# Optimization experiments

Hardware: AMD Instinct MI355X
Metric: run time of the kernel (lower is better)

## Reference

```python
import jax, jax.numpy as jnp
import numpy as np

N = 50000
E = 600000
IN_DIM = 256
OUT_DIM = 128
SCALE = 1.8
K = 2
ALPHA = 0.15
EPS = 1e-12  # matches F.normalize eps


def setup_inputs() -> dict:
    key = jax.random.key(0)
    k1, k2, k3, k4 = jax.random.split(key, 4)
    x = jax.random.normal(k1, (N, IN_DIM), dtype=jnp.float32)
    edge_index = jax.random.randint(k2, (2, E), 0, N, dtype=jnp.int64)
    # nn.Linear params (Kaiming-uniform-ish init scale)
    lim = 1.0 / np.sqrt(IN_DIM)
    W = jax.random.uniform(k3, (OUT_DIM, IN_DIM), dtype=jnp.float32, minval=-lim, maxval=lim)
    b = jax.random.uniform(k4, (OUT_DIM,), dtype=jnp.float32, minval=-lim, maxval=lim)
    return {"x": x, "edge_index": edge_index, "W": W, "b": b}


def _gcn_norm(edge_index, num_nodes):
    # add self loops, symmetric normalization D^-1/2 A D^-1/2
    loops = jnp.arange(num_nodes, dtype=edge_index.dtype)
    row = jnp.concatenate([edge_index[0], loops])  # source
    col = jnp.concatenate([edge_index[1], loops])  # target
    deg = jax.ops.segment_sum(jnp.ones_like(col, dtype=jnp.float32), col,
                              num_segments=num_nodes)
    dinv = jnp.where(deg > 0, jax.lax.rsqrt(deg), 0.0)
    w = dinv[row] * dinv[col]
    return row, col, w


def reference(x, edge_index, W, b):
    # linear
    h = x @ W.T + b  # [N, OUT_DIM]
    # L2 normalize over feature dim, then scale
    nrm = jnp.sqrt(jnp.sum(h * h, axis=1, keepdims=True))
    h = h / jnp.maximum(nrm, EPS) * SCALE
    # APPNP propagation (eval mode: edge dropout disabled)
    row, col, w = _gcn_norm(edge_index, N)
    z = h
    for _ in range(K):
        msg = w[:, None] * z[row]  # gather + weight, [E+N, OUT_DIM]
        agg = jax.ops.segment_sum(msg, col, num_segments=N)
        z = (1.0 - ALPHA) * agg + ALPHA * h
    return z
```

## Files before the change

### kernel.cpp

```cpp
#include <hip/hip_runtime.h>
#include <hip/hip_bf16.h>

#define NNODES 50000
#define IN_DIM 256
#define OUT_DIM 128
#define SCALE 1.8f
#define ALPHA 0.15f
#define DSTRIDE 64

typedef unsigned short ushort_t;
typedef __attribute__((ext_vector_type(8))) _Float16 f16x8;
typedef __attribute__((ext_vector_type(4))) float f32x4;


__device__ __forceinline__ unsigned short f2bf_rne(float f) {
    unsigned int u = __float_as_uint(f);
    unsigned int r = u + 0x7fffu + ((u >> 16) & 1u);
    return (unsigned short)(r >> 16);
}

__device__ __forceinline__ float2 bf2_to_f2(unsigned int p) {
    float2 f;
    f.x = __uint_as_float(p << 16);
    f.y = __uint_as_float(p & 0xffff0000u);
    return f;
}

__device__ __forceinline__ unsigned int f2_to_bf2(float x, float y) {
    return (unsigned int)f2bf_rne(x) | ((unsigned int)f2bf_rne(y) << 16);
}

__device__ __forceinline__ unsigned short f2h(float f) {
    _Float16 h = (_Float16)f;
    return *(unsigned short*)&h;
}


__global__ void init_kernel(const float* __restrict__ W, ushort_t* __restrict__ Whf,
                            int* __restrict__ cnt) {
    int i = blockIdx.x * 256 + threadIdx.x;
    if (i < 50048) cnt[i] = 0;
    if (i < OUT_DIM * IN_DIM) Whf[i] = f2h(W[i]);
}


__global__ void fill_kernel(const int* __restrict__ row, const int* __restrict__ col,
                            int* __restrict__ cnt, int* __restrict__ csr, int E) {
    int e = blockIdx.x * blockDim.x + threadIdx.x;
    if (e < E) {
        int c = col[e];
        int p = atomicAdd(&cnt[c], 1);
        if (p < DSTRIDE) csr[c * DSTRIDE + p] = row[e];
    }
}


#define XPAD 264

__global__ void __launch_bounds__(256, 4) gemm_norm_kernel(
        const float* __restrict__ x, const ushort_t* __restrict__ Whf,
        const float* __restrict__ b, const int* __restrict__ cnt,
        ushort_t* __restrict__ s0b) {
    __shared__ __align__(16) ushort_t xh[64][XPAD];

    const int t = threadIdx.x;
    const int wv = t >> 6;
    const int lane = t & 63;
    const int q = lane >> 4;
    const int c = lane & 15;
    const int rowBase = blockIdx.x * 64;

    f16x8 wf[2][8];
    float bias[2];
    #pragma unroll
    for (int j = 0; j < 2; ++j) {
        const size_t base = (size_t)((2 * wv + j) * 16 + c) * IN_DIM + q * 8;
        #pragma unroll
        for (int kt = 0; kt < 8; ++kt)
            wf[j][kt] = *(const f16x8*)(Whf + base + kt * 32);
        bias[j] = b[(2 * wv + j) * 16 + c];
    }

    #pragma unroll
    for (int it = 0; it < 16; ++it) {
        int s = it * 256 + t;
        int r = s >> 6;
        int ks = (s & 63) * 4;
        int grow = rowBase + r;
        float4 v = make_float4(0.f, 0.f, 0.f, 0.f);
        if (grow < NNODES) v = *(const float4*)(x + (size_t)grow * IN_DIM + ks);
        uint2 p;
        p.x = (unsigned int)f2h(v.x) | ((unsigned int)f2h(v.y) << 16);
        p.y = (unsigned int)f2h(v.z) | ((unsigned int)f2h(v.w) << 16);
        *(uint2*)&xh[r][ks] = p;
    }
    __syncthreads();

    f32x4 acc[4][2];
    #pragma unroll
    for (int m = 0; m < 4; ++m)
        #pragma unroll
        for (int j = 0; j < 2; ++j) {
            acc[m][j][0] = bias[j]; acc[m][j][1] = bias[j];
            acc[m][j][2] = bias[j]; acc[m][j][3] = bias[j];
        }

    #pragma unroll
    for (int kt = 0; kt < 8; ++kt) {
        const int kb = kt * 32 + q * 8;
        #pragma unroll
        for (int m = 0; m < 4; ++m) {
            f16x8 a = *(const f16x8*)&xh[m * 16 + c][kb];
            #pragma unroll
            for (int j = 0; j < 2; ++j)
                acc[m][j] = __builtin_amdgcn_mfma_f32_16x16x32_f16(a, wf[j][kt], acc[m][j], 0, 0, 0);
        }
    }

    float psum[4][4];
    #pragma unroll
    for (int m = 0; m < 4; ++m)
        #pragma unroll
        for (int r = 0; r < 4; ++r)
            psum[m][r] = acc[m][0][r] * acc[m][0][r] + acc[m][1][r] * acc[m][1][r];
    #pragma unroll
    for (int mask = 1; mask < 16; mask <<= 1)
        #pragma unroll
        for (int m = 0; m < 4; ++m)
            #pragma unroll
            for (int r = 0; r < 4; ++r)
                psum[m][r] += __shfl_xor(psum[m][r], mask);

    __syncthreads();
    float* red = (float*)&xh[0][0];
    float* scl = red + 64 * 8;
    if (c == 0) {
        #pragma unroll
        for (int m = 0; m < 4; ++m)
            #pragma unroll
            for (int r = 0; r < 4; ++r)
                red[(m * 16 + q * 4 + r) * 8 + wv] = psum[m][r];
    }
    __syncthreads();
    if (t < 64) {
        float s = red[t * 8 + 0] + red[t * 8 + 1] + red[t * 8 + 2] + red[t * 8 + 3];
        float d = rsqrtf((float)(cnt[rowBase + t] + 1));
        scl[t] = d * SCALE / fmaxf(sqrtf(s), 1e-12f);
    }
    __syncthreads();

    #pragma unroll
    for (int m = 0; m < 4; ++m) {
        #pragma unroll
        for (int r = 0; r < 4; ++r) {
            int lrow = m * 16 + q * 4 + r;
            int grow = rowBase + lrow;
            if (grow < NNODES) {
                float sc = scl[lrow];
                #pragma unroll
                for (int j = 0; j < 2; ++j) {
                    float o = acc[m][j][r] * sc;
                    s0b[(size_t)grow * OUT_DIM + (2 * wv + j) * 16 + c] = f2bf_rne(o);
                }
            }
        }
    }
}


__device__ __forceinline__ void acc_row4(float2* a, uint4 v) {
    float2 f0 = bf2_to_f2(v.x), f1 = bf2_to_f2(v.y);
    float2 f2 = bf2_to_f2(v.z), f3 = bf2_to_f2(v.w);
    a[0].x += f0.x; a[0].y += f0.y;
    a[1].x += f1.x; a[1].y += f1.y;
    a[2].x += f2.x; a[2].y += f2.y;
    a[3].x += f3.x; a[3].y += f3.y;
}

template <int FINAL>
__global__ void __launch_bounds__(256) gather_kernel(
        const int* __restrict__ cnt, const int* __restrict__ csr,
        const unsigned int* __restrict__ sin, const unsigned int* __restrict__ s0,
        unsigned int* __restrict__ sout_b, float* __restrict__ out_f) {
    const int wv = threadIdx.x >> 6;
    const int lane = threadIdx.x & 63;
    const int qd = lane >> 4;
    const int d16 = lane & 15;
    const int c = blockIdx.x * 4 + wv;

    const int deg = cnt[c];
    int n = deg;
    if (n > DSTRIDE) n = DSTRIDE;
    int idx = 0;
    if (lane < n) idx = csr[c * DSTRIDE + lane];

    float2 a[4];
    #pragma unroll
    for (int k = 0; k < 4; ++k) a[k] = make_float2(0.f, 0.f);

    int j = 0;
    for (; j + 8 <= n; j += 8) {
        int r0 = __shfl(idx, j + qd);
        int r1 = __shfl(idx, j + 4 + qd);
        uint4 v0 = *(const uint4*)(sin + (size_t)r0 * 64 + d16 * 4);
        uint4 v1 = *(const uint4*)(sin + (size_t)r1 * 64 + d16 * 4);
        acc_row4(a, v0);
        acc_row4(a, v1);
    }
    for (; j < n; j += 4) {
        int jj = j + qd;
        int r0 = __shfl(idx, (jj < n) ? jj : (n - 1));
        if (jj < n) {
            uint4 v0 = *(const uint4*)(sin + (size_t)r0 * 64 + d16 * 4);
            acc_row4(a, v0);
        }
    }

    #pragma unroll
    for (int k = 0; k < 4; ++k) {
        a[k].x += __shfl_xor(a[k].x, 16);
        a[k].y += __shfl_xor(a[k].y, 16);
        a[k].x += __shfl_xor(a[k].x, 32);
        a[k].y += __shfl_xor(a[k].y, 32);
    }

    if (qd == 0) {
        const float degp1 = (float)(deg + 1);
        uint4 zc4 = *(const uint4*)(sin + (size_t)c * 64 + d16 * 4);
        float2 zc[4];
        zc[0] = bf2_to_f2(zc4.x); zc[1] = bf2_to_f2(zc4.y);
        zc[2] = bf2_to_f2(zc4.z); zc[3] = bf2_to_f2(zc4.w);
        #pragma unroll
        for (int k = 0; k < 4; ++k) {
            a[k].x += zc[k].x;
            a[k].y += zc[k].y;
        }
        if (FINAL) {
            float d = rsqrtf(degp1);
            float gx = (1.0f - ALPHA) * d;
            float gy = ALPHA * sqrtf(degp1);
            uint4 z04 = *(const uint4*)(s0 + (size_t)c * 64 + d16 * 4);
            float2 z0[4];
            z0[0] = bf2_to_f2(z04.x); z0[1] = bf2_to_f2(z04.y);
            z0[2] = bf2_to_f2(z04.z); z0[3] = bf2_to_f2(z04.w);
            float4 o0, o1;
            o0.x = gx * a[0].x + gy * z0[0].x;
            o0.y = gx * a[0].y + gy * z0[0].y;
            o0.z = gx * a[1].x + gy * z0[1].x;
            o0.w = gx * a[1].y + gy * z0[1].y;
            o1.x = gx * a[2].x + gy * z0[2].x;
            o1.y = gx * a[2].y + gy * z0[2].y;
            o1.z = gx * a[3].x + gy * z0[3].x;
            o1.w = gx * a[3].y + gy * z0[3].y;
            float* p = out_f + (size_t)c * 128 + d16 * 8;
            *(float4*)(p) = o0;
            *(float4*)(p + 4) = o1;
        } else {
            float qc = (1.0f - ALPHA) / degp1;
            uint4 w;
            w.x = f2_to_bf2(qc * a[0].x + ALPHA * zc[0].x, qc * a[0].y + ALPHA * zc[0].y);
            w.y = f2_to_bf2(qc * a[1].x + ALPHA * zc[1].x, qc * a[1].y + ALPHA * zc[1].y);
            w.z = f2_to_bf2(qc * a[2].x + ALPHA * zc[2].x, qc * a[2].y + ALPHA * zc[2].y);
            w.w = f2_to_bf2(qc * a[3].x + ALPHA * zc[3].x, qc * a[3].y + ALPHA * zc[3].y);
            *(uint4*)(sout_b + (size_t)c * 64 + d16 * 4) = w;
        }
    }
}

extern "C" void kernel_launch(void* const* d_in, const int* in_sizes, int n_in,
                              void* d_out, int out_size, void* d_ws, size_t ws_size,
                              hipStream_t stream) {
    const float* x  = (const float*)d_in[0];
    const int*   ei = (const int*)d_in[1];
    const float* W  = (const float*)d_in[2];
    const float* b  = (const float*)d_in[3];
    float* out = (float*)d_out;

    int E = in_sizes[1] / 2;
    const int* row = ei;
    const int* col = ei + E;

    unsigned int* s0b = (unsigned int*)d_ws;
    unsigned int* s1b = s0b + (size_t)NNODES * 64;
    int* csr = (int*)(s1b + (size_t)NNODES * 64);
    int* cnt = csr + (size_t)NNODES * DSTRIDE;
    ushort_t* Whf = (ushort_t*)(cnt + 50048);

    init_kernel<<<196, 256, 0, stream>>>(W, Whf, cnt);
    fill_kernel<<<(E + 255) / 256, 256, 0, stream>>>(row, col, cnt, csr, E);
    gemm_norm_kernel<<<(NNODES + 63) / 64, 256, 0, stream>>>(x, Whf, b, cnt, (ushort_t*)s0b);
    gather_kernel<0><<<NNODES / 4, 256, 0, stream>>>(cnt, csr, s0b, s0b, s1b, nullptr);
    gather_kernel<1><<<NNODES / 4, 256, 0, stream>>>(cnt, csr, s1b, s0b, nullptr, out);
}
```

Measured before the change: 196.3 us.

## Fuse CSR fill into GEMM launch, defer degree scaling to gather, use 16-bit CSR

The separate init, fill and GEMM kernels are merged into one launch. Extra blocks build the CSR with atomics while the GEMM blocks run independently, and W is converted to fp16 inline instead of in a pre-pass. Because the GEMM no longer needs the degree counts, the source-side D^-1/2 factor moves into the first gather as a per-neighbour rsqrt of cnt. CSR indices are stored as 16-bit values to halve index traffic, which risks truncation since node ids go up to 50000 (below 65536, so they fit). The cost is an extra cnt load per edge in the first gather.

```diff
diff --git a/kernel.cpp b/kernel.cpp
--- a/kernel.cpp
+++ b/kernel.cpp
@@ -7,6 +7,7 @@
 #define SCALE 1.8f
 #define ALPHA 0.15f
 #define DSTRIDE 64
+#define GEMM_BLOCKS 782
 
 typedef unsigned short ushort_t;
 typedef __attribute__((ext_vector_type(8))) _Float16 f16x8;
@@ -36,32 +37,28 @@
 }
 
 
-__global__ void init_kernel(const float* __restrict__ W, ushort_t* __restrict__ Whf,
-                            int* __restrict__ cnt) {
-    int i = blockIdx.x * 256 + threadIdx.x;
-    if (i < 50048) cnt[i] = 0;
-    if (i < OUT_DIM * IN_DIM) Whf[i] = f2h(W[i]);
-}
-
-
-__global__ void fill_kernel(const int* __restrict__ row, const int* __restrict__ col,
-                            int* __restrict__ cnt, int* __restrict__ csr, int E) {
-    int e = blockIdx.x * blockDim.x + threadIdx.x;
-    if (e < E) {
-        int c = col[e];
-        int p = atomicAdd(&cnt[c], 1);
-        if (p < DSTRIDE) csr[c * DSTRIDE + p] = row[e];
-    }
-}
-
-
 #define XPAD 264
 
-__global__ void __launch_bounds__(256, 4) gemm_norm_kernel(
-        const float* __restrict__ x, const ushort_t* __restrict__ Whf,
-        const float* __restrict__ b, const int* __restrict__ cnt,
-        ushort_t* __restrict__ s0b) {
+__global__ void __launch_bounds__(256, 4) prep_gemm_kernel(
+        const float* __restrict__ x, const float* __restrict__ W,
+        const float* __restrict__ b,
+        const int* __restrict__ row, const int* __restrict__ col, int E,
+        int* __restrict__ cnt, ushort_t* __restrict__ csr16,
+        ushort_t* __restrict__ u0b) {
     __shared__ __align__(16) ushort_t xh[64][XPAD];
+
+    if (blockIdx.x >= GEMM_BLOCKS) {
+        int e0 = ((blockIdx.x - GEMM_BLOCKS) * 256 + threadIdx.x) * 2;
+        if (e0 < E) {
+            int2 rr = *(const int2*)(row + e0);
+            int2 cc = *(const int2*)(col + e0);
+            int p0 = atomicAdd(&cnt[cc.x], 1);
+            if (p0 < DSTRIDE) csr16[(size_t)cc.x * DSTRIDE + p0] = (ushort_t)rr.x;
+            int p1 = atomicAdd(&cnt[cc.y], 1);
+            if (p1 < DSTRIDE) csr16[(size_t)cc.y * DSTRIDE + p1] = (ushort_t)rr.y;
+        }
+        return;
+    }
 
     const int t = threadIdx.x;
     const int wv = t >> 6;
@@ -76,8 +73,16 @@
     for (int j = 0; j < 2; ++j) {
         const size_t base = (size_t)((2 * wv + j) * 16 + c) * IN_DIM + q * 8;
         #pragma unroll
-        for (int kt = 0; kt < 8; ++kt)
-            wf[j][kt] = *(const f16x8*)(Whf + base + kt * 32);
+        for (int kt = 0; kt < 8; ++kt) {
+            float4 w0 = *(const float4*)(W + base + kt * 32);
+            float4 w1 = *(const float4*)(W + base + kt * 32 + 4);
+            f16x8 wp;
+            wp[0] = (_Float16)w0.x; wp[1] = (_Float16)w0.y;
+            wp[2] = (_Float16)w0.z; wp[3] = (_Float16)w0.w;
+            wp[4] = (_Float16)w1.x; wp[5] = (_Float16)w1.y;
+            wp[6] = (_Float16)w1.z; wp[7] = (_Float16)w1.w;
+            wf[j][kt] = wp;
+        }
         bias[j] = b[(2 * wv + j) * 16 + c];
     }
 
@@ -144,8 +149,7 @@
     __syncthreads();
     if (t < 64) {
         float s = red[t * 8 + 0] + red[t * 8 + 1] + red[t * 8 + 2] + red[t * 8 + 3];
-        float d = rsqrtf((float)(cnt[rowBase + t] + 1));
-        scl[t] = d * SCALE / fmaxf(sqrtf(s), 1e-12f);
+        scl[t] = SCALE / fmaxf(sqrtf(s), 1e-12f);
     }
     __syncthreads();
 
@@ -160,7 +164,7 @@
                 #pragma unroll
                 for (int j = 0; j < 2; ++j) {
                     float o = acc[m][j][r] * sc;
-                    s0b[(size_t)grow * OUT_DIM + (2 * wv + j) * 16 + c] = f2bf_rne(o);
+                    u0b[(size_t)grow * OUT_DIM + (2 * wv + j) * 16 + c] = f2bf_rne(o);
                 }
             }
         }
@@ -168,19 +172,10 @@
 }
 
 
-__device__ __forceinline__ void acc_row4(float2* a, uint4 v) {
-    float2 f0 = bf2_to_f2(v.x), f1 = bf2_to_f2(v.y);
-    float2 f2 = bf2_to_f2(v.z), f3 = bf2_to_f2(v.w);
-    a[0].x += f0.x; a[0].y += f0.y;
-    a[1].x += f1.x; a[1].y += f1.y;
-    a[2].x += f2.x; a[2].y += f2.y;
-    a[3].x += f3.x; a[3].y += f3.y;
-}
-
 template <int FINAL>
 __global__ void __launch_bounds__(256) gather_kernel(
-        const int* __restrict__ cnt, const int* __restrict__ csr,
-        const unsigned int* __restrict__ sin, const unsigned int* __restrict__ s0,
+        const int* __restrict__ cnt, const ushort_t* __restrict__ csr16,
+        const unsigned int* __restrict__ sin, const unsigned int* __restrict__ u0,
         unsigned int* __restrict__ sout_b, float* __restrict__ out_f) {
     const int wv = threadIdx.x >> 6;
     const int lane = threadIdx.x & 63;
@@ -192,7 +187,7 @@
     int n = deg;
     if (n > DSTRIDE) n = DSTRIDE;
     int idx = 0;
-    if (lane < n) idx = csr[c * DSTRIDE + lane];
+    if (lane < n) idx = (int)csr16[(size_t)c * DSTRIDE + lane];
 
     float2 a[4];
     #pragma unroll
@@ -202,17 +197,43 @@
     for (; j + 8 <= n; j += 8) {
         int r0 = __shfl(idx, j + qd);
         int r1 = __shfl(idx, j + 4 + qd);
+        float sc0 = 1.0f, sc1 = 1.0f;
+        if (!FINAL) {
+            sc0 = rsqrtf((float)(cnt[r0] + 1));
+            sc1 = rsqrtf((float)(cnt[r1] + 1));
+        }
         uint4 v0 = *(const uint4*)(sin + (size_t)r0 * 64 + d16 * 4);
         uint4 v1 = *(const uint4*)(sin + (size_t)r1 * 64 + d16 * 4);
-        acc_row4(a, v0);
-        acc_row4(a, v1);
+        {
+            float2 f0 = bf2_to_f2(v0.x), f1 = bf2_to_f2(v0.y);
+            float2 f2 = bf2_to_f2(v0.z), f3 = bf2_to_f2(v0.w);
+            a[0].x += sc0 * f0.x; a[0].y += sc0 * f0.y;
+            a[1].x += sc0 * f1.x; a[1].y += sc0 * f1.y;
+            a[2].x += sc0 * f2.x; a[2].y += sc0 * f2.y;
+            a[3].x += sc0 * f3.x; a[3].y += sc0 * f3.y;
+        }
+        {
+            float2 f0 = bf2_to_f2(v1.x), f1 = bf2_to_f2(v1.y);
+            float2 f2 = bf2_to_f2(v1.z), f3 = bf2_to_f2(v1.w);
+            a[0].x += sc1 * f0.x; a[0].y += sc1 * f0.y;
+            a[1].x += sc1 * f1.x; a[1].y += sc1 * f1.y;
+            a[2].x += sc1 * f2.x; a[2].y += sc1 * f2.y;
+            a[3].x += sc1 * f3.x; a[3].y += sc1 * f3.y;
+        }
     }
     for (; j < n; j += 4) {
         int jj = j + qd;
-        int r0 = __shfl(idx, (jj < n) ? jj : (n - 1));
+        int rr = __shfl(idx, (jj < n) ? jj : (n - 1));
         if (jj < n) {
-            uint4 v0 = *(const uint4*)(sin + (size_t)r0 * 64 + d16 * 4);
-            acc_row4(a, v0);
+            float sc = 1.0f;
+            if (!FINAL) sc = rsqrtf((float)(cnt[rr] + 1));
+            uint4 v = *(const uint4*)(sin + (size_t)rr * 64 + d16 * 4);
+            float2 f0 = bf2_to_f2(v.x), f1 = bf2_to_f2(v.y);
+            float2 f2 = bf2_to_f2(v.z), f3 = bf2_to_f2(v.w);
+            a[0].x += sc * f0.x; a[0].y += sc * f0.y;
+            a[1].x += sc * f1.x; a[1].y += sc * f1.y;
+            a[2].x += sc * f2.x; a[2].y += sc * f2.y;
+            a[3].x += sc * f3.x; a[3].y += sc * f3.y;
         }
     }
 
@@ -226,42 +247,47 @@
 
     if (qd == 0) {
         const float degp1 = (float)(deg + 1);
+        const float dc = rsqrtf(degp1);
         uint4 zc4 = *(const uint4*)(sin + (size_t)c * 64 + d16 * 4);
         float2 zc[4];
         zc[0] = bf2_to_f2(zc4.x); zc[1] = bf2_to_f2(zc4.y);
         zc[2] = bf2_to_f2(zc4.z); zc[3] = bf2_to_f2(zc4.w);
-        #pragma unroll
-        for (int k = 0; k < 4; ++k) {
-            a[k].x += zc[k].x;
-            a[k].y += zc[k].y;
-        }
         if (FINAL) {
-            float d = rsqrtf(degp1);
-            float gx = (1.0f - ALPHA) * d;
-            float gy = ALPHA * sqrtf(degp1);
-            uint4 z04 = *(const uint4*)(s0 + (size_t)c * 64 + d16 * 4);
+            #pragma unroll
+            for (int k = 0; k < 4; ++k) {
+                a[k].x += zc[k].x;
+                a[k].y += zc[k].y;
+            }
+            uint4 z04 = *(const uint4*)(u0 + (size_t)c * 64 + d16 * 4);
             float2 z0[4];
             z0[0] = bf2_to_f2(z04.x); z0[1] = bf2_to_f2(z04.y);
             z0[2] = bf2_to_f2(z04.z); z0[3] = bf2_to_f2(z04.w);
+            float gx = (1.0f - ALPHA) * dc;
             float4 o0, o1;
-            o0.x = gx * a[0].x + gy * z0[0].x;
-            o0.y = gx * a[0].y + gy * z0[0].y;
-            o0.z = gx * a[1].x + gy * z0[1].x;
-            o0.w = gx * a[1].y + gy * z0[1].y;
-            o1.x = gx * a[2].x + gy * z0[2].x;
-            o1.y = gx * a[2].y + gy * z0[2].y;
-            o1.z = gx * a[3].x + gy * z0[3].x;
-            o1.w = gx * a[3].y + gy * z0[3].y;
+            o0.x = gx * a[0].x + ALPHA * z0[0].x;
+            o0.y = gx * a[0].y + ALPHA * z0[0].y;
+            o0.z = gx * a[1].x + ALPHA * z0[1].x;
+            o0.w = gx * a[1].y + ALPHA * z0[1].y;
+            o1.x = gx * a[2].x + ALPHA * z0[2].x;
+            o1.y = gx * a[2].y + ALPHA * z0[2].y;
+            o1.z = gx * a[3].x + ALPHA * z0[3].x;
+            o1.w = gx * a[3].y + ALPHA * z0[3].y;
             float* p = out_f + (size_t)c * 128 + d16 * 8;
             *(float4*)(p) = o0;
             *(float4*)(p + 4) = o1;
         } else {
-            float qc = (1.0f - ALPHA) / degp1;
+            #pragma unroll
+            for (int k = 0; k < 4; ++k) {
+                a[k].x += dc * zc[k].x;
+                a[k].y += dc * zc[k].y;
+            }
+            float qc = (1.0f - ALPHA) * dc * dc;
+            float ac = ALPHA * dc;
             uint4 w;
-            w.x = f2_to_bf2(qc * a[0].x + ALPHA * zc[0].x, qc * a[0].y + ALPHA * zc[0].y);
-            w.y = f2_to_bf2(qc * a[1].x + ALPHA * zc[1].x, qc * a[1].y + ALPHA * zc[1].y);
-            w.z = f2_to_bf2(qc * a[2].x + ALPHA * zc[2].x, qc * a[2].y + ALPHA * zc[2].y);
-            w.w = f2_to_bf2(qc * a[3].x + ALPHA * zc[3].x, qc * a[3].y + ALPHA * zc[3].y);
+            w.x = f2_to_bf2(qc * a[0].x + ac * zc[0].x, qc * a[0].y + ac * zc[0].y);
+            w.y = f2_to_bf2(qc * a[1].x + ac * zc[1].x, qc * a[1].y + ac * zc[1].y);
+            w.z = f2_to_bf2(qc * a[2].x + ac * zc[2].x, qc * a[2].y + ac * zc[2].y);
+            w.w = f2_to_bf2(qc * a[3].x + ac * zc[3].x, qc * a[3].y + ac * zc[3].y);
             *(uint4*)(sout_b + (size_t)c * 64 + d16 * 4) = w;
         }
     }
@@ -280,15 +306,17 @@
     const int* row = ei;
     const int* col = ei + E;
 
-    unsigned int* s0b = (unsigned int*)d_ws;
-    unsigned int* s1b = s0b + (size_t)NNODES * 64;
-    int* csr = (int*)(s1b + (size_t)NNODES * 64);
-    int* cnt = csr + (size_t)NNODES * DSTRIDE;
-    ushort_t* Whf = (ushort_t*)(cnt + 50048);
-
-    init_kernel<<<196, 256, 0, stream>>>(W, Whf, cnt);
-    fill_kernel<<<(E + 255) / 256, 256, 0, stream>>>(row, col, cnt, csr, E);
-    gemm_norm_kernel<<<(NNODES + 63) / 64, 256, 0, stream>>>(x, Whf, b, cnt, (ushort_t*)s0b);
-    gather_kernel<0><<<NNODES / 4, 256, 0, stream>>>(cnt, csr, s0b, s0b, s1b, nullptr);
-    gather_kernel<1><<<NNODES / 4, 256, 0, stream>>>(cnt, csr, s1b, s0b, nullptr, out);
-}
+    unsigned int* u0b = (unsigned int*)d_ws;
+    unsigned int* s1b = u0b + (size_t)NNODES * 64;
+    int* cnt = (int*)(s1b + (size_t)NNODES * 64);
+    ushort_t* csr16 = (ushort_t*)(cnt + 50048);
+
+    hipMemsetAsync(cnt, 0, 50048 * sizeof(int), stream);
+
+    int fillBlocks = (E + 511) / 512;
+    prep_gemm_kernel<<<GEMM_BLOCKS + fillBlocks, 256, 0, stream>>>(
+        x, W, b, row, col, E, cnt, csr16, (ushort_t*)u0b);
+
+    gather_kernel<0><<<NNODES / 4, 256, 0, stream>>>(cnt, csr16, u0b, u0b, s1b, nullptr);
+    gather_kernel<1><<<NNODES / 4, 256, 0, stream>>>(cnt, csr16, s1b, u0b, nullptr, out);
+}
```

After: 198.6 us. About the same (+1.2%).

## Map one node per 16 lanes in gather, compress CSR to 16-bit indices

Applied to the files above, without the earlier changes.

The gather kernel now assigns one destination node to each group of 16 lanes instead of one node per 64-lane wave. This removes the cross-quarter shuffle reduction and the idle lanes in the epilogue, and up to eight neighbor rows are loaded in flight before accumulating. The CSR neighbor list is stored as 16-bit indices, which halves index traffic; this relies on node ids fitting in 16 bits, and 50000 does fit. The fill kernel processes two edges per thread with vector loads. Nodes with high degree now serialize their neighbors within 16 lanes, which may increase imbalance between lane groups.

```diff
diff --git a/kernel.cpp b/kernel.cpp
--- a/kernel.cpp
+++ b/kernel.cpp
@@ -45,12 +45,15 @@
 
 
 __global__ void fill_kernel(const int* __restrict__ row, const int* __restrict__ col,
-                            int* __restrict__ cnt, int* __restrict__ csr, int E) {
-    int e = blockIdx.x * blockDim.x + threadIdx.x;
-    if (e < E) {
-        int c = col[e];
-        int p = atomicAdd(&cnt[c], 1);
-        if (p < DSTRIDE) csr[c * DSTRIDE + p] = row[e];
+                            int* __restrict__ cnt, ushort_t* __restrict__ csr16, int E) {
+    int e0 = (blockIdx.x * 256 + threadIdx.x) * 2;
+    if (e0 < E) {
+        int2 rr = *(const int2*)(row + e0);
+        int2 cc = *(const int2*)(col + e0);
+        int p0 = atomicAdd(&cnt[cc.x], 1);
+        if (p0 < DSTRIDE) csr16[(size_t)cc.x * DSTRIDE + p0] = (ushort_t)rr.x;
+        int p1 = atomicAdd(&cnt[cc.y], 1);
+        if (p1 < DSTRIDE) csr16[(size_t)cc.y * DSTRIDE + p1] = (ushort_t)rr.y;
     }
 }
 
@@ -179,91 +182,82 @@
 
 template <int FINAL>
 __global__ void __launch_bounds__(256) gather_kernel(
-        const int* __restrict__ cnt, const int* __restrict__ csr,
+        const int* __restrict__ cnt, const ushort_t* __restrict__ csr16,
         const unsigned int* __restrict__ sin, const unsigned int* __restrict__ s0,
         unsigned int* __restrict__ sout_b, float* __restrict__ out_f) {
-    const int wv = threadIdx.x >> 6;
-    const int lane = threadIdx.x & 63;
-    const int qd = lane >> 4;
-    const int d16 = lane & 15;
-    const int c = blockIdx.x * 4 + wv;
-
-    const int deg = cnt[c];
-    int n = deg;
-    if (n > DSTRIDE) n = DSTRIDE;
-    int idx = 0;
-    if (lane < n) idx = csr[c * DSTRIDE + lane];
+    const int tid = threadIdx.x;
+    const int d16 = tid & 15;
+    const int q16 = tid & 0x30;
+    const int c = blockIdx.x * 16 + (tid >> 4);
+
+    int deg = cnt[c];
+    if (deg > DSTRIDE) deg = DSTRIDE;
+
+    uint4 zc4 = *(const uint4*)(sin + (size_t)c * 64 + d16 * 4);
+    uint4 z04 = zc4;
+    if (FINAL) z04 = *(const uint4*)(s0 + (size_t)c * 64 + d16 * 4);
 
     float2 a[4];
     #pragma unroll
     for (int k = 0; k < 4; ++k) a[k] = make_float2(0.f, 0.f);
 
-    int j = 0;
-    for (; j + 8 <= n; j += 8) {
-        int r0 = __shfl(idx, j + qd);
-        int r1 = __shfl(idx, j + 4 + qd);
-        uint4 v0 = *(const uint4*)(sin + (size_t)r0 * 64 + d16 * 4);
-        uint4 v1 = *(const uint4*)(sin + (size_t)r1 * 64 + d16 * 4);
-        acc_row4(a, v0);
-        acc_row4(a, v1);
-    }
-    for (; j < n; j += 4) {
-        int jj = j + qd;
-        int r0 = __shfl(idx, (jj < n) ? jj : (n - 1));
-        if (jj < n) {
-            uint4 v0 = *(const uint4*)(sin + (size_t)r0 * 64 + d16 * 4);
-            acc_row4(a, v0);
-        }
-    }
-
+    for (int w = 0; w < deg; w += 16) {
+        int nw = deg - w;
+        if (nw > 16) nw = 16;
+        int idx = (int)csr16[(size_t)c * DSTRIDE + w + (d16 < nw ? d16 : nw - 1)];
+        for (int bb = 0; bb < nw; bb += 8) {
+            int nb = nw - bb;
+            if (nb > 8) nb = 8;
+            uint4 vv[8];
+            #pragma unroll
+            for (int k = 0; k < 8; ++k) {
+                if (k < nb) {
+                    int r = __shfl(idx, q16 + bb + k);
+                    vv[k] = *(const uint4*)(sin + (size_t)r * 64 + d16 * 4);
+                }
+            }
+            #pragma unroll
+            for (int k = 0; k < 8; ++k)
+                if (k < nb) acc_row4(a, vv[k]);
+        }
+    }
+
+    const float degp1 = (float)(deg + 1);
+    float2 zc[4];
+    zc[0] = bf2_to_f2(zc4.x); zc[1] = bf2_to_f2(zc4.y);
+    zc[2] = bf2_to_f2(zc4.z); zc[3] = bf2_to_f2(zc4.w);
     #pragma unroll
     for (int k = 0; k < 4; ++k) {
-        a[k].x += __shfl_xor(a[k].x, 16);
-        a[k].y += __shfl_xor(a[k].y, 16);
-        a[k].x += __shfl_xor(a[k].x, 32);
-        a[k].y += __shfl_xor(a[k].y, 32);
-    }
-
-    if (qd == 0) {
-        const float degp1 = (float)(deg + 1);
-        uint4 zc4 = *(const uint4*)(sin + (size_t)c * 64 + d16 * 4);
-        float2 zc[4];
-        zc[0] = bf2_to_f2(zc4.x); zc[1] = bf2_to_f2(zc4.y);
-        zc[2] = bf2_to_f2(zc4.z); zc[3] = bf2_to_f2(zc4.w);
-        #pragma unroll
-        for (int k = 0; k < 4; ++k) {
-            a[k].x += zc[k].x;
-            a[k].y += zc[k].y;
-        }
-        if (FINAL) {
-            float d = rsqrtf(degp1);
-            float gx = (1.0f - ALPHA) * d;
-            float gy = ALPHA * sqrtf(degp1);
-            uint4 z04 = *(const uint4*)(s0 + (size_t)c * 64 + d16 * 4);
-            float2 z0[4];
-            z0[0] = bf2_to_f2(z04.x); z0[1] = bf2_to_f2(z04.y);
-            z0[2] = bf2_to_f2(z04.z); z0[3] = bf2_to_f2(z04.w);
-            float4 o0, o1;
-            o0.x = gx * a[0].x + gy * z0[0].x;
-            o0.y = gx * a[0].y + gy * z0[0].y;
-            o0.z = gx * a[1].x + gy * z0[1].x;
-            o0.w = gx * a[1].y + gy * z0[1].y;
-            o1.x = gx * a[2].x + gy * z0[2].x;
-            o1.y = gx * a[2].y + gy * z0[2].y;
-            o1.z = gx * a[3].x + gy * z0[3].x;
-            o1.w = gx * a[3].y + gy * z0[3].y;
-            float* p = out_f + (size_t)c * 128 + d16 * 8;
-            *(float4*)(p) = o0;
-            *(float4*)(p + 4) = o1;
-        } else {
-            float qc = (1.0f - ALPHA) / degp1;
-            uint4 w;
-            w.x = f2_to_bf2(qc * a[0].x + ALPHA * zc[0].x, qc * a[0].y + ALPHA * zc[0].y);
-            w.y = f2_to_bf2(qc * a[1].x + ALPHA * zc[1].x, qc * a[1].y + ALPHA * zc[1].y);
-            w.z = f2_to_bf2(qc * a[2].x + ALPHA * zc[2].x, qc * a[2].y + ALPHA * zc[2].y);
-            w.w = f2_to_bf2(qc * a[3].x + ALPHA * zc[3].x, qc * a[3].y + ALPHA * zc[3].y);
-            *(uint4*)(sout_b + (size_t)c * 64 + d16 * 4) = w;
-        }
+        a[k].x += zc[k].x;
+        a[k].y += zc[k].y;
+    }
+    if (FINAL) {
+        float dc = rsqrtf(degp1);
+        float gx = (1.0f - ALPHA) * dc;
+        float gy = ALPHA * sqrtf(degp1);
+        float2 z0[4];
+        z0[0] = bf2_to_f2(z04.x); z0[1] = bf2_to_f2(z04.y);
+        z0[2] = bf2_to_f2(z04.z); z0[3] = bf2_to_f2(z04.w);
+        float4 o0, o1;
+        o0.x = gx * a[0].x + gy * z0[0].x;
+        o0.y = gx * a[0].y + gy * z0[0].y;
+        o0.z = gx * a[1].x + gy * z0[1].x;
+        o0.w = gx * a[1].y + gy * z0[1].y;
+        o1.x = gx * a[2].x + gy * z0[2].x;
+        o1.y = gx * a[2].y + gy * z0[2].y;
+        o1.z = gx * a[3].x + gy * z0[3].x;
+        o1.w = gx * a[3].y + gy * z0[3].y;
+        float* p = out_f + (size_t)c * 128 + d16 * 8;
+        *(float4*)(p) = o0;
+        *(float4*)(p + 4) = o1;
+    } else {
+        float qc = (1.0f - ALPHA) / degp1;
+        uint4 wout;
+        wout.x = f2_to_bf2(qc * a[0].x + ALPHA * zc[0].x, qc * a[0].y + ALPHA * zc[0].y);
+        wout.y = f2_to_bf2(qc * a[1].x + ALPHA * zc[1].x, qc * a[1].y + ALPHA * zc[1].y);
+        wout.z = f2_to_bf2(qc * a[2].x + ALPHA * zc[2].x, qc * a[2].y + ALPHA * zc[2].y);
+        wout.w = f2_to_bf2(qc * a[3].x + ALPHA * zc[3].x, qc * a[3].y + ALPHA * zc[3].y);
+        *(uint4*)(sout_b + (size_t)c * 64 + d16 * 4) = wout;
     }
 }
 
@@ -282,13 +276,13 @@
 
     unsigned int* s0b = (unsigned int*)d_ws;
     unsigned int* s1b = s0b + (size_t)NNODES * 64;
-    int* csr = (int*)(s1b + (size_t)NNODES * 64);
-    int* cnt = csr + (size_t)NNODES * DSTRIDE;
-    ushort_t* Whf = (ushort_t*)(cnt + 50048);
+    int* cnt = (int*)(s1b + (size_t)NNODES * 64);
+    ushort_t* csr16 = (ushort_t*)(cnt + 50048);
+    ushort_t* Whf = csr16 + (size_t)NNODES * DSTRIDE;
 
     init_kernel<<<196, 256, 0, stream>>>(W, Whf, cnt);
-    fill_kernel<<<(E + 255) / 256, 256, 0, stream>>>(row, col, cnt, csr, E);
+    fill_kernel<<<(E / 2 + 255) / 256, 256, 0, stream>>>(row, col, cnt, csr16, E);
     gemm_norm_kernel<<<(NNODES + 63) / 64, 256, 0, stream>>>(x, Whf, b, cnt, (ushort_t*)s0b);
-    gather_kernel<0><<<NNODES / 4, 256, 0, stream>>>(cnt, csr, s0b, s0b, s1b, nullptr);
-    gather_kernel<1><<<NNODES / 4, 256, 0, stream>>>(cnt, csr, s1b, s0b, nullptr, out);
-}
+    gather_kernel<0><<<NNODES / 16, 256, 0, stream>>>(cnt, csr16, s0b, s0b, s1b, nullptr);
+    gather_kernel<1><<<NNODES / 16, 256, 0, stream>>>(cnt, csr16, s1b, s0b, nullptr, out);
+}
```

Measured after the change: 204.3 us. +4.1%, slower.

## Use 16-bit CSR indices, slice the fill by destination, and drop the init kernel

Applied to the files above, without the earlier changes.

Neighbor indices in the padded CSR are now stored as ushort instead of int, which halves index traffic in the fill and in both gather passes; this relies on N being below 65536. The fill kernel becomes a grid-stride loop over a fixed set of blocks. Each block handles only one of 8 destination-node slices, which should localize the atomics and scattered CSR writes, at the cost of every slice re-reading the full col array. The separate init kernel is removed: the counters are cleared with hipMemsetAsync, and W is converted to fp16 directly inside the GEMM kernel's register loads.

```diff
diff --git a/kernel.cpp b/kernel.cpp
--- a/kernel.cpp
+++ b/kernel.cpp
@@ -7,6 +7,8 @@
 #define SCALE 1.8f
 #define ALPHA 0.15f
 #define DSTRIDE 64
+#define FILL_BLOCKS 1024
+#define SLICE_N 6250
 
 typedef unsigned short ushort_t;
 typedef __attribute__((ext_vector_type(8))) _Float16 f16x8;
@@ -36,21 +38,25 @@
 }
 
 
-__global__ void init_kernel(const float* __restrict__ W, ushort_t* __restrict__ Whf,
-                            int* __restrict__ cnt) {
-    int i = blockIdx.x * 256 + threadIdx.x;
-    if (i < 50048) cnt[i] = 0;
-    if (i < OUT_DIM * IN_DIM) Whf[i] = f2h(W[i]);
-}
-
-
 __global__ void fill_kernel(const int* __restrict__ row, const int* __restrict__ col,
-                            int* __restrict__ cnt, int* __restrict__ csr, int E) {
-    int e = blockIdx.x * blockDim.x + threadIdx.x;
-    if (e < E) {
-        int c = col[e];
-        int p = atomicAdd(&cnt[c], 1);
-        if (p < DSTRIDE) csr[c * DSTRIDE + p] = row[e];
+                            int* __restrict__ cnt, ushort_t* __restrict__ csr16, int E) {
+    const int slice = blockIdx.x & 7;
+    const int gidx = blockIdx.x >> 3;
+    const int lo = slice * SLICE_N;
+    const int hi = lo + SLICE_N;
+    const int GSTRIDE = (FILL_BLOCKS / 8) * 512;
+    for (int e0 = (gidx * 256 + (int)threadIdx.x) * 2; e0 < E; e0 += GSTRIDE) {
+        int2 cc = *(const int2*)(col + e0);
+        if (cc.x >= lo && cc.x < hi) {
+            int r = row[e0];
+            int p = atomicAdd(&cnt[cc.x], 1);
+            if (p < DSTRIDE) csr16[(size_t)cc.x * DSTRIDE + p] = (ushort_t)r;
+        }
+        if (cc.y >= lo && cc.y < hi) {
+            int r = row[e0 + 1];
+            int p = atomicAdd(&cnt[cc.y], 1);
+            if (p < DSTRIDE) csr16[(size_t)cc.y * DSTRIDE + p] = (ushort_t)r;
+        }
     }
 }
 
@@ -58,7 +64,7 @@
 #define XPAD 264
 
 __global__ void __launch_bounds__(256, 4) gemm_norm_kernel(
-        const float* __restrict__ x, const ushort_t* __restrict__ Whf,
+        const float* __restrict__ x, const float* __restrict__ W,
         const float* __restrict__ b, const int* __restrict__ cnt,
         ushort_t* __restrict__ s0b) {
     __shared__ __align__(16) ushort_t xh[64][XPAD];
@@ -76,8 +82,16 @@
     for (int j = 0; j < 2; ++j) {
         const size_t base = (size_t)((2 * wv + j) * 16 + c) * IN_DIM + q * 8;
         #pragma unroll
-        for (int kt = 0; kt < 8; ++kt)
-            wf[j][kt] = *(const f16x8*)(Whf + base + kt * 32);
+        for (int kt = 0; kt < 8; ++kt) {
+            float4 w0 = *(const float4*)(W + base + kt * 32);
+            float4 w1 = *(const float4*)(W + base + kt * 32 + 4);
+            f16x8 wp;
+            wp[0] = (_Float16)w0.x; wp[1] = (_Float16)w0.y;
+            wp[2] = (_Float16)w0.z; wp[3] = (_Float16)w0.w;
+            wp[4] = (_Float16)w1.x; wp[5] = (_Float16)w1.y;
+            wp[6] = (_Float16)w1.z; wp[7] = (_Float16)w1.w;
+            wf[j][kt] = wp;
+        }
         bias[j] = b[(2 * wv + j) * 16 + c];
     }
 
@@ -179,7 +193,7 @@
 
 template <int FINAL>
 __global__ void __launch_bounds__(256) gather_kernel(
-        const int* __restrict__ cnt, const int* __restrict__ csr,
+        const int* __restrict__ cnt, const ushort_t* __restrict__ csr16,
         const unsigned int* __restrict__ sin, const unsigned int* __restrict__ s0,
         unsigned int* __restrict__ sout_b, float* __restrict__ out_f) {
     const int wv = threadIdx.x >> 6;
@@ -192,7 +206,7 @@
     int n = deg;
     if (n > DSTRIDE) n = DSTRIDE;
     int idx = 0;
-    if (lane < n) idx = csr[c * DSTRIDE + lane];
+    if (lane < n) idx = (int)csr16[(size_t)c * DSTRIDE + lane];
 
     float2 a[4];
     #pragma unroll
@@ -209,10 +223,10 @@
     }
     for (; j < n; j += 4) {
         int jj = j + qd;
-        int r0 = __shfl(idx, (jj < n) ? jj : (n - 1));
+        int rr = __shfl(idx, (jj < n) ? jj : (n - 1));
         if (jj < n) {
-            uint4 v0 = *(const uint4*)(sin + (size_t)r0 * 64 + d16 * 4);
-            acc_row4(a, v0);
+            uint4 v = *(const uint4*)(sin + (size_t)rr * 64 + d16 * 4);
+            acc_row4(a, v);
         }
     }
 
@@ -236,8 +250,8 @@
             a[k].y += zc[k].y;
         }
         if (FINAL) {
-            float d = rsqrtf(degp1);
-            float gx = (1.0f - ALPHA) * d;
+            float dc = rsqrtf(degp1);
+            float gx = (1.0f - ALPHA) * dc;
             float gy = ALPHA * sqrtf(degp1);
             uint4 z04 = *(const uint4*)(s0 + (size_t)c * 64 + d16 * 4);
             float2 z0[4];
@@ -282,13 +296,12 @@
 
     unsigned int* s0b = (unsigned int*)d_ws;
     unsigned int* s1b = s0b + (size_t)NNODES * 64;
-    int* csr = (int*)(s1b + (size_t)NNODES * 64);
-    int* cnt = csr + (size_t)NNODES * DSTRIDE;
-    ushort_t* Whf = (ushort_t*)(cnt + 50048);
-
-    init_kernel<<<196, 256, 0, stream>>>(W, Whf, cnt);
-    fill_kernel<<<(E + 255) / 256, 256, 0, stream>>>(row, col, cnt, csr, E);
-    gemm_norm_kernel<<<(NNODES + 63) / 64, 256, 0, stream>>>(x, Whf, b, cnt, (ushort_t*)s0b);
-    gather_kernel<0><<<NNODES / 4, 256, 0, stream>>>(cnt, csr, s0b, s0b, s1b, nullptr);
-    gather_kernel<1><<<NNODES / 4, 256, 0, stream>>>(cnt, csr, s1b, s0b, nullptr, out);
-}
+    int* cnt = (int*)(s1b + (size_t)NNODES * 64);
+    ushort_t* csr16 = (ushort_t*)(cnt + 50048);
+
+    hipMemsetAsync(cnt, 0, 50048 * sizeof(int), stream);
+    fill_kernel<<<FILL_BLOCKS, 256, 0, stream>>>(row, col, cnt, csr16, E);
+    gemm_norm_kernel<<<(NNODES + 63) / 64, 256, 0, stream>>>(x, W, b, cnt, (ushort_t*)s0b);
+    gather_kernel<0><<<NNODES / 4, 256, 0, stream>>>(cnt, csr16, s0b, s0b, s1b, nullptr);
+    gather_kernel<1><<<NNODES / 4, 256, 0, stream>>>(cnt, csr16, s1b, s0b, nullptr, out);
+}
```

Result: slower. 209.7 us (+6.9%).
